# Kernel optimization log

Measured on AMD Instinct MI355X. Metric: run time of the kernel, lower is better.

Reference implementation:

```python
import jax, jax.numpy as jnp
import numpy as np

N_NODES = 100000
N_EDGES = 1600000
N_GRAPHS = 1024
N_FEAT = 128
HID = 64
N_CLASSES = 16
N_CENT = 3  # centroids per class


def setup_inputs() -> dict:
    key = jax.random.key(0)
    ks = jax.random.split(key, 8)
    x = jax.random.normal(ks[0], (N_NODES, N_FEAT), dtype=jnp.float32)
    edge_index = jax.random.randint(ks[1], (2, N_EDGES), 0, N_NODES, dtype=jnp.int64)
    batch = jnp.sort(jax.random.randint(ks[2], (N_NODES,), 0, N_GRAPHS, dtype=jnp.int64))
    s = 1.0 / np.sqrt(N_FEAT)
    W1 = jax.random.normal(ks[3], (N_FEAT, HID), dtype=jnp.float32) * s
    W2 = jax.random.normal(ks[4], (HID, HID), dtype=jnp.float32) * (1.0 / np.sqrt(HID))
    W3 = jax.random.normal(ks[5], (HID, HID), dtype=jnp.float32) * (1.0 / np.sqrt(HID))
    b1 = jnp.zeros((HID,), jnp.float32)
    b2 = jnp.zeros((HID,), jnp.float32)
    b3 = jnp.zeros((HID,), jnp.float32)
    centroids = jax.random.normal(ks[6], (N_CLASSES * N_CENT, HID), dtype=jnp.float32)
    reject_bias = jnp.zeros((1,), jnp.float32)
    return {"x": x, "edge_index": edge_index, "batch": batch,
            "W1": W1, "b1": b1, "W2": W2, "b2": b2, "W3": W3, "b3": b3,
            "centroids": centroids, "reject_bias": reject_bias}


def _gcn_conv(x, W, b, src, dst, norm, n_nodes):
    # PyG GCNConv: out[dst] = sum_e norm_e * (x[src_e] @ W), + bias
    h = x @ W                      # [N, out]
    msg = h[src] * norm[:, None]   # [E+N, out] gather + scale
    out = jax.ops.segment_sum(msg, dst, num_segments=n_nodes)
    return out + b


def reference(x, edge_index, batch, W1, b1, W2, b2, W3, b3, centroids, reject_bias):
    n = x.shape[0]
    loops = jnp.arange(n, dtype=edge_index.dtype)
    src = jnp.concatenate([edge_index[0], loops])
    dst = jnp.concatenate([edge_index[1], loops])
    # symmetric normalization on A + I
    deg = jax.ops.segment_sum(jnp.ones_like(dst, dtype=x.dtype), dst, num_segments=n)
    dinv = jax.lax.rsqrt(jnp.maximum(deg, 1.0))
    norm = dinv[src] * dinv[dst]

    h = jax.nn.relu(_gcn_conv(x, W1, b1, src, dst, norm, n))  # dropout is identity at eval
    h = jax.nn.relu(_gcn_conv(h, W2, b2, src, dst, norm, n))
    h = _gcn_conv(h, W3, b3, src, dst, norm, n)

    # global mean pool over graphs in the batch
    summ = jax.ops.segment_sum(h, batch, num_segments=N_GRAPHS)          # [G, HID]
    cnt = jax.ops.segment_sum(jnp.ones((n,), h.dtype), batch, num_segments=N_GRAPHS)
    emb = summ / jnp.maximum(cnt, 1.0)[:, None]

    # centroid distance head: squared euclidean to all class centroids
    d = (jnp.sum(emb * emb, -1, keepdims=True)
         - 2.0 * emb @ centroids.T
         + jnp.sum(centroids * centroids, -1))                           # [G, 16*3]
    d_pc = jnp.min(d.reshape(-1, N_CLASSES, N_CENT), axis=-1)            # [G, 16]
    class_logits = -d_pc
    reject_logit = jnp.min(d_pc, axis=-1, keepdims=True) - reject_bias   # [G, 1]
    return jnp.concatenate([class_logits, reject_logit], axis=-1)        # [G, 17]
```

## Files before the change

### kernel.cpp

```cpp
#include <hip/hip_runtime.h>

#define HID 64
#define NCLS 16
#define NCENT 3
#define NCENTS (NCLS * NCENT)
#define BSHIFT 9
#define BINW (1 << BSHIFT)
#define NBINMAX 256
#define CHUNK 4096
#define EPT (CHUNK / 256)
#define NU 8

static inline int ceil_div(int a, int b) { return (a + b - 1) / b; }

__device__ inline unsigned short f2bf(float f) {
    unsigned int u = __float_as_uint(f);
    return (unsigned short)((u + 0x7FFFu + ((u >> 16) & 1u)) >> 16);
}
__device__ inline unsigned int pack2bf(float lo, float hi) {
    return (unsigned int)f2bf(lo) | ((unsigned int)f2bf(hi) << 16);
}
__device__ inline float bf2f(unsigned short h) {
    return __uint_as_float(((unsigned int)h) << 16);
}
__device__ inline float bflo(unsigned int u) { return __uint_as_float(u << 16); }
__device__ inline float bfhi(unsigned int u) { return __uint_as_float(u & 0xFFFF0000u); }

typedef short bf16x8 __attribute__((ext_vector_type(8)));
typedef float f32x4 __attribute__((ext_vector_type(4)));


__global__ void k_count(const int* __restrict__ dst, int* __restrict__ binCnt,
                        int E, int nbins) {
    __shared__ int c[NBINMAX];
    for (int i = threadIdx.x; i < nbins; i += 256) c[i] = 0;
    __syncthreads();
    int e = blockIdx.x * CHUNK + threadIdx.x;
#pragma unroll
    for (int j = 0; j < EPT; j++, e += 256)
        if (e < E) atomicAdd(&c[dst[e] >> BSHIFT], 1);
    __syncthreads();
    for (int i = threadIdx.x; i < nbins; i += 256)
        if (c[i] > 0) atomicAdd(&binCnt[i], c[i]);
}

__global__ void k_binoff(const int* __restrict__ binCnt, int* __restrict__ binBase,
                         int nbins, int E) {
    __shared__ int ts[NBINMAX];
    int t = threadIdx.x;
    int v = (t < nbins) ? binCnt[t] : 0;
    ts[t] = v;
    __syncthreads();
    for (int off = 1; off < NBINMAX; off <<= 1) {
        int x = (t >= off) ? ts[t - off] : 0;
        __syncthreads();
        ts[t] += x;
        __syncthreads();
    }
    if (t < nbins) binBase[t] = ts[t] - v;
    if (t == 0) binBase[nbins] = E;
}

__global__ __launch_bounds__(256) void k_bin(const int* __restrict__ src,
                                             const int* __restrict__ dst,
                                             const int* __restrict__ binBase,
                                             int* __restrict__ binCur,
                                             int2* __restrict__ binned,
                                             int E, int nbins) {
    __shared__ int cnt[NBINMAX], off[NBINMAX], gbase[NBINMAX];
    __shared__ int2 stage[CHUNK];
    const int c0 = blockIdx.x * CHUNK;
    const int tid = threadIdx.x;
    cnt[tid] = 0;
    __syncthreads();
    int sv[EPT], dv[EPT];
#pragma unroll
    for (int j = 0; j < EPT; j++) {
        int e = c0 + j * 256 + tid;
        dv[j] = -1;
        if (e < E) {
            sv[j] = src[e];
            dv[j] = dst[e];
            atomicAdd(&cnt[dv[j] >> BSHIFT], 1);
        }
    }
    __syncthreads();
    off[tid] = cnt[tid];
    __syncthreads();
    for (int o = 1; o < NBINMAX; o <<= 1) {
        int x = (tid >= o) ? off[tid - o] : 0;
        __syncthreads();
        off[tid] += x;
        __syncthreads();
    }
    int excl = off[tid] - cnt[tid];
    __syncthreads();
    off[tid] = excl;
    gbase[tid] = (tid < nbins && cnt[tid] > 0) ? atomicAdd(&binCur[tid], cnt[tid]) : 0;
    cnt[tid] = 0;
    __syncthreads();
#pragma unroll
    for (int j = 0; j < EPT; j++)
        if (dv[j] >= 0) {
            int b = dv[j] >> BSHIFT;
            int pos = off[b] + atomicAdd(&cnt[b], 1);
            stage[pos] = make_int2(sv[j], dv[j]);
        }
    __syncthreads();
    int tot = min(CHUNK, E - c0);
    for (int i = tid; i < tot; i += 256) {
        int2 v = stage[i];
        int b = v.y >> BSHIFT;
        binned[binBase[b] + gbase[b] + (i - off[b])] = v;
    }
}

__global__ __launch_bounds__(256) void k_fillc2(const int2* __restrict__ binned,
                                                const int* __restrict__ binBase,
                                                int* __restrict__ col,
                                                int* __restrict__ rs_out,
                                                int* __restrict__ deg_out,
                                                float* __restrict__ dinv_out, int N) {
    __shared__ int c[BINW];
    __shared__ int rsl[BINW];
    __shared__ int ts[256];
    int b = blockIdx.x;
    int s = binBase[b], e = binBase[b + 1];
    int n0 = b << BSHIFT;
    int t = threadIdx.x;
    c[2 * t] = 0; c[2 * t + 1] = 0;
    __syncthreads();
    for (int i = s + t; i < e; i += 256)
        atomicAdd(&c[binned[i].y - n0], 1);
    __syncthreads();
    int v0 = c[2 * t], v1 = c[2 * t + 1];
    ts[t] = v0 + v1;
    __syncthreads();
    for (int off = 1; off < 256; off <<= 1) {
        int x = (t >= off) ? ts[t - off] : 0;
        __syncthreads();
        ts[t] += x;
        __syncthreads();
    }
    int base = binBase[b] + ts[t] - (v0 + v1);
    rsl[2 * t] = base;
    rsl[2 * t + 1] = base + v0;
    int n = n0 + 2 * t;
    if (n < N) {
        deg_out[n] = v0; rs_out[n] = base;
        dinv_out[n] = rsqrtf((float)(v0 + 1));
    }
    if (n + 1 < N) {
        deg_out[n + 1] = v1; rs_out[n + 1] = base + v0;
        dinv_out[n + 1] = rsqrtf((float)(v1 + 1));
    }
    c[2 * t] = 0; c[2 * t + 1] = 0;
    __syncthreads();
    for (int i = s + t; i < e; i += 256) {
        int2 v = binned[i];
        int lo = v.y - n0;
        int pos = rsl[lo] + atomicAdd(&c[lo], 1);
        col[pos] = v.x;
    }
}


__device__ void wprep_one(const float* __restrict__ W, unsigned short* __restrict__ Wh,
                          unsigned short* __restrict__ Wl, int K) {
    for (int idx = threadIdx.x; idx < K * 64; idx += 256) {
        int k = idx >> 6, colc = idx & 63;
        float f = W[idx];
        unsigned short h = f2bf(f);
        unsigned short lo = f2bf(f - bf2f(h));
        int kt = k >> 5, kin = k & 31, ct = colc >> 4;
        int ln = ((kin >> 3) << 4) | (colc & 15);
        int o = (((kt * 4 + ct) * 64) + ln) * 8 + (kin & 7);
        Wh[o] = h; Wl[o] = lo;
    }
}

__global__ void k_wprep(const float* __restrict__ W1, const float* __restrict__ W2,
                        const float* __restrict__ W3,
                        unsigned short* __restrict__ W1h, unsigned short* __restrict__ W1l,
                        unsigned short* __restrict__ W2h, unsigned short* __restrict__ W2l,
                        unsigned short* __restrict__ W3h, unsigned short* __restrict__ W3l) {
    if (blockIdx.x == 0) wprep_one(W1, W1h, W1l, 128);
    else if (blockIdx.x == 1) wprep_one(W2, W2h, W2l, 64);
    else wprep_one(W3, W3h, W3l, 64);
}


template <int K, bool BF>
__global__ __launch_bounds__(256) void k_gemm_mfma(const void* __restrict__ Ain,
                                                   const unsigned short* __restrict__ Wh,
                                                   const unsigned short* __restrict__ Wl,
                                                   unsigned short* __restrict__ out,
                                                   const float* __restrict__ dinv, int N) {
    const int lane = threadIdx.x & 63;
    const int wave = threadIdx.x >> 6;
    const int row0 = blockIdx.x * 64 + wave * 16;
    int arow = row0 + (lane & 15);
    if (arow > N - 1) arow = N - 1;
    const int kb = (lane >> 4) * 8;

    f32x4 acc[4] = {};

#pragma unroll
    for (int kt = 0; kt < K / 32; ++kt) {
        bf16x8 ah, al;
        if (BF) {
            ah = *(const bf16x8*)((const unsigned short*)Ain + (size_t)arow * K + kt * 32 + kb);
        } else {
            const float* ap = (const float*)Ain + (size_t)arow * K + kt * 32 + kb;
            float4 f0 = *(const float4*)ap;
            float4 f1 = *(const float4*)(ap + 4);
            float fv[8] = {f0.x, f0.y, f0.z, f0.w, f1.x, f1.y, f1.z, f1.w};
#pragma unroll
            for (int j = 0; j < 8; ++j) {
                unsigned short h = f2bf(fv[j]);
                ah[j] = (short)h;
                al[j] = (short)f2bf(fv[j] - bf2f(h));
            }
        }
#pragma unroll
        for (int ct = 0; ct < 4; ++ct) {
            const size_t wo = ((size_t)(kt * 4 + ct) * 64 + lane) * 8;
            bf16x8 wh = *(const bf16x8*)(Wh + wo);
            bf16x8 wl = *(const bf16x8*)(Wl + wo);
            acc[ct] = __builtin_amdgcn_mfma_f32_16x16x32_bf16(ah, wh, acc[ct], 0, 0, 0);
            if (!BF)
                acc[ct] = __builtin_amdgcn_mfma_f32_16x16x32_bf16(al, wh, acc[ct], 0, 0, 0);
            acc[ct] = __builtin_amdgcn_mfma_f32_16x16x32_bf16(ah, wl, acc[ct], 0, 0, 0);
        }
    }

    const int rb = row0 + (lane >> 4) * 4;
    const int cb = lane & 15;
#pragma unroll
    for (int i = 0; i < 4; ++i) {
        int row = rb + i;
        if (row < N) {
            float d = dinv[row];
#pragma unroll
            for (int ct = 0; ct < 4; ++ct)
                out[(size_t)row * HID + ct * 16 + cb] = f2bf(d * acc[ct][i]);
        }
    }
}


__global__ void k_agg(const unsigned short* __restrict__ tin,
                      unsigned short* __restrict__ out,
                      const int* __restrict__ rs, const int* __restrict__ deg,
                      const int* __restrict__ col,
                      const float* __restrict__ dinv, const float* __restrict__ bias,
                      int N, int relu) {
    int node = (blockIdx.x * blockDim.x + threadIdx.x) >> 3;
    int l = threadIdx.x & 7;
    if (node >= N) return;
    float di = dinv[node];
    uint4 tb = ((const uint4*)(tin + (size_t)node * HID))[l];
    float a0 = bflo(tb.x), a1 = bfhi(tb.x);
    float a2 = bflo(tb.y), a3 = bfhi(tb.y);
    float a4 = bflo(tb.z), a5 = bfhi(tb.z);
    float a6 = bflo(tb.w), a7 = bfhi(tb.w);

    int beg = rs[node];
    int cnt = deg[node];
    int last = beg + cnt - 1;
    for (int e = 0; e < cnt; e += NU) {
        int sv[NU];
#pragma unroll
        for (int j = 0; j < NU; j++) {
            int idx = beg + e + j;
            sv[j] = col[idx < last ? idx : last];
        }
        uint4 vv[NU];
#pragma unroll
        for (int j = 0; j < NU; j++) vv[j] = ((const uint4*)(tin + (size_t)sv[j] * HID))[l];
#pragma unroll
        for (int j = 0; j < NU; j++) {
            a0 += bflo(vv[j].x); a1 += bfhi(vv[j].x);
            a2 += bflo(vv[j].y); a3 += bfhi(vv[j].y);
            a4 += bflo(vv[j].z); a5 += bfhi(vv[j].z);
            a6 += bflo(vv[j].w); a7 += bfhi(vv[j].w);
        }
    }
    int pad = (NU - (cnt & (NU - 1))) & (NU - 1);
    if (cnt > 0 && pad > 0) {
        float fp = (float)pad;
        uint4 vl = ((const uint4*)(tin + (size_t)col[last] * HID))[l];
        a0 = fmaf(-fp, bflo(vl.x), a0); a1 = fmaf(-fp, bfhi(vl.x), a1);
        a2 = fmaf(-fp, bflo(vl.y), a2); a3 = fmaf(-fp, bfhi(vl.y), a3);
        a4 = fmaf(-fp, bflo(vl.z), a4); a5 = fmaf(-fp, bfhi(vl.z), a5);
        a6 = fmaf(-fp, bflo(vl.w), a6); a7 = fmaf(-fp, bfhi(vl.w), a7);
    }
    float4 b0 = ((const float4*)bias)[2 * l];
    float4 b1 = ((const float4*)bias)[2 * l + 1];
    a0 = fmaf(di, a0, b0.x); a1 = fmaf(di, a1, b0.y);
    a2 = fmaf(di, a2, b0.z); a3 = fmaf(di, a3, b0.w);
    a4 = fmaf(di, a4, b1.x); a5 = fmaf(di, a5, b1.y);
    a6 = fmaf(di, a6, b1.z); a7 = fmaf(di, a7, b1.w);
    if (relu) {
        a0 = fmaxf(a0, 0.f); a1 = fmaxf(a1, 0.f); a2 = fmaxf(a2, 0.f); a3 = fmaxf(a3, 0.f);
        a4 = fmaxf(a4, 0.f); a5 = fmaxf(a5, 0.f); a6 = fmaxf(a6, 0.f); a7 = fmaxf(a7, 0.f);
    }
    uint4 o;
    o.x = pack2bf(a0, a1); o.y = pack2bf(a2, a3);
    o.z = pack2bf(a4, a5); o.w = pack2bf(a6, a7);
    ((uint4*)(out + (size_t)node * HID))[l] = o;
}


__global__ void k_pool_head(const unsigned short* __restrict__ h,
                            const int* __restrict__ batch,
                            const float* __restrict__ cent, const float* __restrict__ rbias,
                            float* __restrict__ out, int N) {
    int g = blockIdx.x;
    int lo = 0, hi = N;
    while (lo < hi) { int mid = (lo + hi) >> 1; if (batch[mid] < g) lo = mid + 1; else hi = mid; }
    int s = lo;
    lo = 0; hi = N;
    while (lo < hi) { int mid = (lo + hi) >> 1; if (batch[mid] < g + 1) lo = mid + 1; else hi = mid; }
    int e = lo;

    __shared__ float part[4][HID];
    __shared__ float embS[HID];
    __shared__ float dS[NCENTS];
    __shared__ float dpcS[NCLS];

    int lane = threadIdx.x & 63, wid = threadIdx.x >> 6;
    float acc = 0.0f;
    for (int i = s + wid; i < e; i += 4) acc += bf2f(h[(size_t)i * HID + lane]);
    part[wid][lane] = acc;
    __syncthreads();
    if (wid == 0) {
        float v = part[0][lane] + part[1][lane] + part[2][lane] + part[3][lane];
        embS[lane] = v / fmaxf((float)(e - s), 1.0f);
    }
    __syncthreads();
    if (threadIdx.x < NCENTS) {
        const float* c = cent + threadIdx.x * HID;
        float d = 0.0f;
        for (int k = 0; k < HID; k++) { float df = embS[k] - c[k]; d = fmaf(df, df, d); }
        dS[threadIdx.x] = d;
    }
    __syncthreads();
    if (threadIdx.x < NCLS) {
        float m = fminf(dS[threadIdx.x * 3],
                        fminf(dS[threadIdx.x * 3 + 1], dS[threadIdx.x * 3 + 2]));
        dpcS[threadIdx.x] = m;
        out[g * (NCLS + 1) + threadIdx.x] = -m;
    }
    __syncthreads();
    if (threadIdx.x == 0) {
        float m = dpcS[0];
        for (int i = 1; i < NCLS; i++) m = fminf(m, dpcS[i]);
        out[g * (NCLS + 1) + NCLS] = m - rbias[0];
    }
}


extern "C" void kernel_launch(void* const* d_in, const int* in_sizes, int n_in,
                              void* d_out, int out_size, void* d_ws, size_t ws_size,
                              hipStream_t stream) {
    const float* x    = (const float*)d_in[0];
    const int*   ei   = (const int*)d_in[1];
    const int*   bat  = (const int*)d_in[2];
    const float* W1   = (const float*)d_in[3];
    const float* b1   = (const float*)d_in[4];
    const float* W2   = (const float*)d_in[5];
    const float* b2   = (const float*)d_in[6];
    const float* W3   = (const float*)d_in[7];
    const float* b3   = (const float*)d_in[8];
    const float* cent = (const float*)d_in[9];
    const float* rb   = (const float*)d_in[10];
    float* out = (float*)d_out;

    const int N = in_sizes[0] / 128;
    const int E = in_sizes[1] / 2;
    const int nbins = (N + BINW - 1) >> BSHIFT;

    char* p = (char*)d_ws;
    unsigned short* A  = (unsigned short*)p; p += (size_t)N * HID * 2;
    unsigned short* Bb = (unsigned short*)p; p += (size_t)N * HID * 2;
    int2*  binned = (int2*)p;  p += (size_t)E * 8;
    int*   col    = (int*)p;   p += (size_t)E * 4;
    float* dinv   = (float*)p; p += (size_t)N * 4;
    int*   rs     = (int*)p;   p += (size_t)N * 4;
    int*   deg    = (int*)p;   p += (size_t)N * 4;
    int*   binBase= (int*)p;   p += (NBINMAX + 2) * 4;
    int*   binCnt = (int*)p;   p += NBINMAX * 4;
    int*   binCur = (int*)p;   p += NBINMAX * 4;
    p = (char*)(((uintptr_t)p + 15) & ~(uintptr_t)15);
    unsigned short* W1h = (unsigned short*)p; p += 8192 * 2;
    unsigned short* W1l = (unsigned short*)p; p += 8192 * 2;
    unsigned short* W2h = (unsigned short*)p; p += 4096 * 2;
    unsigned short* W2l = (unsigned short*)p; p += 4096 * 2;
    unsigned short* W3h = (unsigned short*)p; p += 4096 * 2;
    unsigned short* W3l = (unsigned short*)p; p += 4096 * 2;

    hipMemsetAsync(binCnt, 0, 2 * NBINMAX * 4, stream);

    k_wprep<<<3, 256, 0, stream>>>(W1, W2, W3, W1h, W1l, W2h, W2l, W3h, W3l);

    k_count<<<ceil_div(E, CHUNK), 256, 0, stream>>>(ei + E, binCnt, E, nbins);
    k_binoff<<<1, 256, 0, stream>>>(binCnt, binBase, nbins, E);
    k_bin<<<ceil_div(E, CHUNK), 256, 0, stream>>>(ei, ei + E, binBase, binCur, binned, E, nbins);
    k_fillc2<<<nbins, 256, 0, stream>>>(binned, binBase, col, rs, deg, dinv, N);

    k_gemm_mfma<128, false><<<ceil_div(N, 64), 256, 0, stream>>>(x, W1h, W1l, A, dinv, N);
    k_agg<<<ceil_div(N * 8, 256), 256, 0, stream>>>(A, Bb, rs, deg, col, dinv, b1, N, 1);
    k_gemm_mfma<64, true><<<ceil_div(N, 64), 256, 0, stream>>>(Bb, W2h, W2l, A, dinv, N);
    k_agg<<<ceil_div(N * 8, 256), 256, 0, stream>>>(A, Bb, rs, deg, col, dinv, b2, N, 1);
    k_gemm_mfma<64, true><<<ceil_div(N, 64), 256, 0, stream>>>(Bb, W3h, W3l, A, dinv, N);
    k_agg<<<ceil_div(N * 8, 256), 256, 0, stream>>>(A, Bb, rs, deg, col, dinv, b3, N, 0);

    k_pool_head<<<1024, 256, 0, stream>>>(Bb, bat, cent, rb, out, N);
}
```

Before: 331.5 us.

## Fuse aggregation with next-layer MFMA GEMM and coalesce neighbor index loads

The layer-1 and layer-2 aggregation kernels now also run the next layer's 64x64 bf16 MFMA transform. The aggregated rows are staged in shared memory, so the separate GEMM kernels and their round trip of the hidden activations through global memory go away. Neighbor indices are now loaded once per 8-lane group and broadcast with shuffles instead of each lane loading all 8. The weight-prep work is folded into extra blocks of the edge-count kernel to save a launch. In exchange, each fused block handles only 32 nodes and waits at a barrier, which can leave the gather poorly balanced when node degrees vary.

```diff
diff --git a/kernel.cpp b/kernel.cpp
--- a/kernel.cpp
+++ b/kernel.cpp
@@ -30,8 +30,35 @@
 typedef float f32x4 __attribute__((ext_vector_type(4)));
 
 
-__global__ void k_count(const int* __restrict__ dst, int* __restrict__ binCnt,
-                        int E, int nbins) {
+__device__ void wprep_one(const float* __restrict__ W, unsigned short* __restrict__ Wh,
+                          unsigned short* __restrict__ Wl, int K) {
+    for (int idx = threadIdx.x; idx < K * 64; idx += 256) {
+        int k = idx >> 6, colc = idx & 63;
+        float f = W[idx];
+        unsigned short h = f2bf(f);
+        unsigned short lo = f2bf(f - bf2f(h));
+        int kt = k >> 5, kin = k & 31, ct = colc >> 4;
+        int ln = ((kin >> 3) << 4) | (colc & 15);
+        int o = (((kt * 4 + ct) * 64) + ln) * 8 + (kin & 7);
+        Wh[o] = h; Wl[o] = lo;
+    }
+}
+
+
+__global__ void k_count_w(const int* __restrict__ dst, int* __restrict__ binCnt,
+                          int E, int nbins,
+                          const float* __restrict__ W1, const float* __restrict__ W2,
+                          const float* __restrict__ W3,
+                          unsigned short* __restrict__ W1h, unsigned short* __restrict__ W1l,
+                          unsigned short* __restrict__ W2h, unsigned short* __restrict__ W2l,
+                          unsigned short* __restrict__ W3h, unsigned short* __restrict__ W3l) {
+    if (blockIdx.x >= gridDim.x - 3) {
+        int w = blockIdx.x - (gridDim.x - 3);
+        if (w == 0) wprep_one(W1, W1h, W1l, 128);
+        else if (w == 1) wprep_one(W2, W2h, W2l, 64);
+        else wprep_one(W3, W3h, W3l, 64);
+        return;
+    }
     __shared__ int c[NBINMAX];
     for (int i = threadIdx.x; i < nbins; i += 256) c[i] = 0;
     __syncthreads();
@@ -165,33 +192,8 @@
 }
 
 
-__device__ void wprep_one(const float* __restrict__ W, unsigned short* __restrict__ Wh,
-                          unsigned short* __restrict__ Wl, int K) {
-    for (int idx = threadIdx.x; idx < K * 64; idx += 256) {
-        int k = idx >> 6, colc = idx & 63;
-        float f = W[idx];
-        unsigned short h = f2bf(f);
-        unsigned short lo = f2bf(f - bf2f(h));
-        int kt = k >> 5, kin = k & 31, ct = colc >> 4;
-        int ln = ((kin >> 3) << 4) | (colc & 15);
-        int o = (((kt * 4 + ct) * 64) + ln) * 8 + (kin & 7);
-        Wh[o] = h; Wl[o] = lo;
-    }
-}
-
-__global__ void k_wprep(const float* __restrict__ W1, const float* __restrict__ W2,
-                        const float* __restrict__ W3,
-                        unsigned short* __restrict__ W1h, unsigned short* __restrict__ W1l,
-                        unsigned short* __restrict__ W2h, unsigned short* __restrict__ W2l,
-                        unsigned short* __restrict__ W3h, unsigned short* __restrict__ W3l) {
-    if (blockIdx.x == 0) wprep_one(W1, W1h, W1l, 128);
-    else if (blockIdx.x == 1) wprep_one(W2, W2h, W2l, 64);
-    else wprep_one(W3, W3h, W3l, 64);
-}
-
-
-template <int K, bool BF>
-__global__ __launch_bounds__(256) void k_gemm_mfma(const void* __restrict__ Ain,
+template <int K>
+__global__ __launch_bounds__(256) void k_gemm_mfma(const float* __restrict__ Ain,
                                                    const unsigned short* __restrict__ Wh,
                                                    const unsigned short* __restrict__ Wl,
                                                    unsigned short* __restrict__ out,
@@ -208,19 +210,15 @@
 #pragma unroll
     for (int kt = 0; kt < K / 32; ++kt) {
         bf16x8 ah, al;
-        if (BF) {
-            ah = *(const bf16x8*)((const unsigned short*)Ain + (size_t)arow * K + kt * 32 + kb);
-        } else {
-            const float* ap = (const float*)Ain + (size_t)arow * K + kt * 32 + kb;
-            float4 f0 = *(const float4*)ap;
-            float4 f1 = *(const float4*)(ap + 4);
-            float fv[8] = {f0.x, f0.y, f0.z, f0.w, f1.x, f1.y, f1.z, f1.w};
-#pragma unroll
-            for (int j = 0; j < 8; ++j) {
-                unsigned short h = f2bf(fv[j]);
-                ah[j] = (short)h;
-                al[j] = (short)f2bf(fv[j] - bf2f(h));
-            }
+        const float* ap = Ain + (size_t)arow * K + kt * 32 + kb;
+        float4 f0 = *(const float4*)ap;
+        float4 f1 = *(const float4*)(ap + 4);
+        float fv[8] = {f0.x, f0.y, f0.z, f0.w, f1.x, f1.y, f1.z, f1.w};
+#pragma unroll
+        for (int j = 0; j < 8; ++j) {
+            unsigned short h = f2bf(fv[j]);
+            ah[j] = (short)h;
+            al[j] = (short)f2bf(fv[j] - bf2f(h));
         }
 #pragma unroll
         for (int ct = 0; ct < 4; ++ct) {
@@ -228,8 +226,7 @@
             bf16x8 wh = *(const bf16x8*)(Wh + wo);
             bf16x8 wl = *(const bf16x8*)(Wl + wo);
             acc[ct] = __builtin_amdgcn_mfma_f32_16x16x32_bf16(ah, wh, acc[ct], 0, 0, 0);
-            if (!BF)
-                acc[ct] = __builtin_amdgcn_mfma_f32_16x16x32_bf16(al, wh, acc[ct], 0, 0, 0);
+            acc[ct] = __builtin_amdgcn_mfma_f32_16x16x32_bf16(al, wh, acc[ct], 0, 0, 0);
             acc[ct] = __builtin_amdgcn_mfma_f32_16x16x32_bf16(ah, wl, acc[ct], 0, 0, 0);
         }
     }
@@ -249,32 +246,42 @@
 }
 
 
-__global__ void k_agg(const unsigned short* __restrict__ tin,
-                      unsigned short* __restrict__ out,
-                      const int* __restrict__ rs, const int* __restrict__ deg,
-                      const int* __restrict__ col,
-                      const float* __restrict__ dinv, const float* __restrict__ bias,
-                      int N, int relu) {
-    int node = (blockIdx.x * blockDim.x + threadIdx.x) >> 3;
-    int l = threadIdx.x & 7;
-    if (node >= N) return;
-    float di = dinv[node];
-    uint4 tb = ((const uint4*)(tin + (size_t)node * HID))[l];
+__global__ __launch_bounds__(256) void k_aggf(const unsigned short* __restrict__ tin,
+                                              unsigned short* __restrict__ tout,
+                                              const int* __restrict__ rs,
+                                              const int* __restrict__ deg,
+                                              const int* __restrict__ col,
+                                              const float* __restrict__ dinv,
+                                              const float* __restrict__ bias,
+                                              const unsigned short* __restrict__ Wh,
+                                              const unsigned short* __restrict__ Wl,
+                                              int N) {
+    __shared__ unsigned int tl[32][36];
+    const int tid = threadIdx.x;
+    const int lane = tid & 63;
+    const int wave = tid >> 6;
+    const int group = tid >> 3;
+    const int l = tid & 7;
+    int node = blockIdx.x * 32 + group;
+    int cnode = node < N ? node : N - 1;
+
+    float di = dinv[cnode];
+    uint4 tb = ((const uint4*)(tin + (size_t)cnode * HID))[l];
     float a0 = bflo(tb.x), a1 = bfhi(tb.x);
     float a2 = bflo(tb.y), a3 = bfhi(tb.y);
     float a4 = bflo(tb.z), a5 = bfhi(tb.z);
     float a6 = bflo(tb.w), a7 = bfhi(tb.w);
 
-    int beg = rs[node];
-    int cnt = deg[node];
+    int beg = rs[cnode];
+    int cnt = deg[cnode];
     int last = beg + cnt - 1;
+    const int gbase = lane & 56;
     for (int e = 0; e < cnt; e += NU) {
+        int idx = beg + e + l;
+        int cv = col[idx < last ? idx : last];
         int sv[NU];
 #pragma unroll
-        for (int j = 0; j < NU; j++) {
-            int idx = beg + e + j;
-            sv[j] = col[idx < last ? idx : last];
-        }
+        for (int j = 0; j < NU; j++) sv[j] = __shfl(cv, gbase + j, 64);
         uint4 vv[NU];
 #pragma unroll
         for (int j = 0; j < NU; j++) vv[j] = ((const uint4*)(tin + (size_t)sv[j] * HID))[l];
@@ -297,14 +304,104 @@
     }
     float4 b0 = ((const float4*)bias)[2 * l];
     float4 b1 = ((const float4*)bias)[2 * l + 1];
+    a0 = fmaxf(fmaf(di, a0, b0.x), 0.f); a1 = fmaxf(fmaf(di, a1, b0.y), 0.f);
+    a2 = fmaxf(fmaf(di, a2, b0.z), 0.f); a3 = fmaxf(fmaf(di, a3, b0.w), 0.f);
+    a4 = fmaxf(fmaf(di, a4, b1.x), 0.f); a5 = fmaxf(fmaf(di, a5, b1.y), 0.f);
+    a6 = fmaxf(fmaf(di, a6, b1.z), 0.f); a7 = fmaxf(fmaf(di, a7, b1.w), 0.f);
+
+    uint4 o;
+    o.x = pack2bf(a0, a1); o.y = pack2bf(a2, a3);
+    o.z = pack2bf(a4, a5); o.w = pack2bf(a6, a7);
+    *(uint4*)&tl[group][4 * l] = o;
+    __syncthreads();
+
+    const int row0 = (wave >> 1) * 16;
+    const int ctb = (wave & 1) * 2;
+    const int arow = row0 + (lane & 15);
+    const int am = lane >> 4;
+
+    f32x4 acc[2] = {};
+#pragma unroll
+    for (int kt = 0; kt < 2; ++kt) {
+        bf16x8 ah = *(const bf16x8*)&tl[arow][kt * 16 + 4 * am];
+#pragma unroll
+        for (int c = 0; c < 2; ++c) {
+            const size_t wo = ((size_t)(kt * 4 + ctb + c) * 64 + lane) * 8;
+            bf16x8 wh = *(const bf16x8*)(Wh + wo);
+            bf16x8 wl = *(const bf16x8*)(Wl + wo);
+            acc[c] = __builtin_amdgcn_mfma_f32_16x16x32_bf16(ah, wh, acc[c], 0, 0, 0);
+            acc[c] = __builtin_amdgcn_mfma_f32_16x16x32_bf16(ah, wl, acc[c], 0, 0, 0);
+        }
+    }
+
+    const int rb = row0 + (lane >> 4) * 4;
+    const int cb = lane & 15;
+#pragma unroll
+    for (int i = 0; i < 4; ++i) {
+        int gnode = blockIdx.x * 32 + rb + i;
+        if (gnode < N) {
+            float d2 = dinv[gnode];
+#pragma unroll
+            for (int c = 0; c < 2; ++c)
+                tout[(size_t)gnode * HID + (ctb + c) * 16 + cb] = f2bf(d2 * acc[c][i]);
+        }
+    }
+}
+
+
+__global__ void k_agg(const unsigned short* __restrict__ tin,
+                      unsigned short* __restrict__ out,
+                      const int* __restrict__ rs, const int* __restrict__ deg,
+                      const int* __restrict__ col,
+                      const float* __restrict__ dinv, const float* __restrict__ bias,
+                      int N) {
+    int node = (blockIdx.x * blockDim.x + threadIdx.x) >> 3;
+    int l = threadIdx.x & 7;
+    if (node >= N) return;
+    int lane = threadIdx.x & 63;
+    float di = dinv[node];
+    uint4 tb = ((const uint4*)(tin + (size_t)node * HID))[l];
+    float a0 = bflo(tb.x), a1 = bfhi(tb.x);
+    float a2 = bflo(tb.y), a3 = bfhi(tb.y);
+    float a4 = bflo(tb.z), a5 = bfhi(tb.z);
+    float a6 = bflo(tb.w), a7 = bfhi(tb.w);
+
+    int beg = rs[node];
+    int cnt = deg[node];
+    int last = beg + cnt - 1;
+    const int gbase = lane & 56;
+    for (int e = 0; e < cnt; e += NU) {
+        int idx = beg + e + l;
+        int cv = col[idx < last ? idx : last];
+        int sv[NU];
+#pragma unroll
+        for (int j = 0; j < NU; j++) sv[j] = __shfl(cv, gbase + j, 64);
+        uint4 vv[NU];
+#pragma unroll
+        for (int j = 0; j < NU; j++) vv[j] = ((const uint4*)(tin + (size_t)sv[j] * HID))[l];
+#pragma unroll
+        for (int j = 0; j < NU; j++) {
+            a0 += bflo(vv[j].x); a1 += bfhi(vv[j].x);
+            a2 += bflo(vv[j].y); a3 += bfhi(vv[j].y);
+            a4 += bflo(vv[j].z); a5 += bfhi(vv[j].z);
+            a6 += bflo(vv[j].w); a7 += bfhi(vv[j].w);
+        }
+    }
+    int pad = (NU - (cnt & (NU - 1))) & (NU - 1);
+    if (cnt > 0 && pad > 0) {
+        float fp = (float)pad;
+        uint4 vl = ((const uint4*)(tin + (size_t)col[last] * HID))[l];
+        a0 = fmaf(-fp, bflo(vl.x), a0); a1 = fmaf(-fp, bfhi(vl.x), a1);
+        a2 = fmaf(-fp, bflo(vl.y), a2); a3 = fmaf(-fp, bfhi(vl.y), a3);
+        a4 = fmaf(-fp, bflo(vl.z), a4); a5 = fmaf(-fp, bfhi(vl.z), a5);
+        a6 = fmaf(-fp, bflo(vl.w), a6); a7 = fmaf(-fp, bfhi(vl.w), a7);
+    }
+    float4 b0 = ((const float4*)bias)[2 * l];
+    float4 b1 = ((const float4*)bias)[2 * l + 1];
     a0 = fmaf(di, a0, b0.x); a1 = fmaf(di, a1, b0.y);
     a2 = fmaf(di, a2, b0.z); a3 = fmaf(di, a3, b0.w);
     a4 = fmaf(di, a4, b1.x); a5 = fmaf(di, a5, b1.y);
     a6 = fmaf(di, a6, b1.z); a7 = fmaf(di, a7, b1.w);
-    if (relu) {
-        a0 = fmaxf(a0, 0.f); a1 = fmaxf(a1, 0.f); a2 = fmaxf(a2, 0.f); a3 = fmaxf(a3, 0.f);
-        a4 = fmaxf(a4, 0.f); a5 = fmaxf(a5, 0.f); a6 = fmaxf(a6, 0.f); a7 = fmaxf(a7, 0.f);
-    }
     uint4 o;
     o.x = pack2bf(a0, a1); o.y = pack2bf(a2, a3);
     o.z = pack2bf(a4, a5); o.w = pack2bf(a6, a7);
@@ -382,8 +479,8 @@
     const int nbins = (N + BINW - 1) >> BSHIFT;
 
     char* p = (char*)d_ws;
-    unsigned short* A  = (unsigned short*)p; p += (size_t)N * HID * 2;
-    unsigned short* Bb = (unsigned short*)p; p += (size_t)N * HID * 2;
+    unsigned short* T0 = (unsigned short*)p; p += (size_t)N * HID * 2;
+    unsigned short* T1 = (unsigned short*)p; p += (size_t)N * HID * 2;
     int2*  binned = (int2*)p;  p += (size_t)E * 8;
     int*   col    = (int*)p;   p += (size_t)E * 4;
     float* dinv   = (float*)p; p += (size_t)N * 4;
@@ -402,19 +499,17 @@
 
     hipMemsetAsync(binCnt, 0, 2 * NBINMAX * 4, stream);
 
-    k_wprep<<<3, 256, 0, stream>>>(W1, W2, W3, W1h, W1l, W2h, W2l, W3h, W3l);
-
-    k_count<<<ceil_div(E, CHUNK), 256, 0, stream>>>(ei + E, binCnt, E, nbins);
+    const int nEB = ceil_div(E, CHUNK);
+    k_count_w<<<nEB + 3, 256, 0, stream>>>(ei + E, binCnt, E, nbins,
+                                           W1, W2, W3, W1h, W1l, W2h, W2l, W3h, W3l);
     k_binoff<<<1, 256, 0, stream>>>(binCnt, binBase, nbins, E);
-    k_bin<<<ceil_div(E, CHUNK), 256, 0, stream>>>(ei, ei + E, binBase, binCur, binned, E, nbins);
+    k_bin<<<nEB, 256, 0, stream>>>(ei, ei + E, binBase, binCur, binned, E, nbins);
     k_fillc2<<<nbins, 256, 0, stream>>>(binned, binBase, col, rs, deg, dinv, N);
 
-    k_gemm_mfma<128, false><<<ceil_div(N, 64), 256, 0, stream>>>(x, W1h, W1l, A, dinv, N);
-    k_agg<<<ceil_div(N * 8, 256), 256, 0, stream>>>(A, Bb, rs, deg, col, dinv, b1, N, 1);
-    k_gemm_mfma<64, true><<<ceil_div(N, 64), 256, 0, stream>>>(Bb, W2h, W2l, A, dinv, N);
-    k_agg<<<ceil_div(N * 8, 256), 256, 0, stream>>>(A, Bb, rs, deg, col, dinv, b2, N, 1);
-    k_gemm_mfma<64, true><<<ceil_div(N, 64), 256, 0, stream>>>(Bb, W3h, W3l, A, dinv, N);
-    k_agg<<<ceil_div(N * 8, 256), 256, 0, stream>>>(A, Bb, rs, deg, col, dinv, b3, N, 0);
-
-    k_pool_head<<<1024, 256, 0, stream>>>(Bb, bat, cent, rb, out, N);
-}
+    k_gemm_mfma<128><<<ceil_div(N, 64), 256, 0, stream>>>(x, W1h, W1l, T0, dinv, N);
+    k_aggf<<<ceil_div(N, 32), 256, 0, stream>>>(T0, T1, rs, deg, col, dinv, b1, W2h, W2l, N);
+    k_aggf<<<ceil_div(N, 32), 256, 0, stream>>>(T1, T0, rs, deg, col, dinv, b2, W3h, W3l, N);
+    k_agg<<<ceil_div(N * 8, 256), 256, 0, stream>>>(T0, T1, rs, deg, col, dinv, b3, N);
+
+    k_pool_head<<<1024, 256, 0, stream>>>(T1, bat, cent, rb, out, N);
+}
```

Measured after the change: 307.4 us, median of 2. 7.3% less time.
